# Kernel tuning notes

Measured on AMD Instinct MI355X. Metric: run time of the kernel, lower is better.

Reference implementation:

```python
import jax, jax.numpy as jnp
import numpy as np

BETA = 5.5
MEM_FILLED = 25  # number of occupied slots per class; remaining slots are zero (empty)


def setup_inputs() -> dict:
    key = jax.random.key(0)
    ks = jax.random.split(key, 7)
    C, M, D = 1000, 50, 1024
    mem = jax.random.normal(ks[0], (C, M, D), jnp.float32)
    # emulate a partially-filled memory bank: slots >= MEM_FILLED are empty (all-zero rows)
    mem = mem * (jnp.arange(M)[None, :, None] < MEM_FILLED)
    return {
        "img_feat": jax.random.normal(ks[1], (1, D), jnp.float32),
        "image_feature_memory": mem,
        "fixed_global_feat_vanilla": jax.random.normal(ks[2], (C, 1, D), jnp.float32),
        "global_bias": 0.01 * jax.random.normal(ks[3], (C, D), jnp.float32),
        "global_bias_key": 0.01 * jax.random.normal(ks[4], (C, D), jnp.float32),
        "global_bias_value": 0.01 * jax.random.normal(ks[5], (C, D), jnp.float32),
        "global_ffn_bias": 0.01 * jax.random.normal(ks[6], (C, D), jnp.float32),
        "logit_scale": jnp.asarray(np.log(100.0), dtype=jnp.float32),
    }


def _l2norm(x, axis=-1):
    return x / jnp.linalg.norm(x, axis=axis, keepdims=True)


def reference(img_feat, image_feature_memory, fixed_global_feat_vanilla,
              global_bias, global_bias_key, global_bias_value,
              global_ffn_bias, logit_scale):
    # DualMem.get_image_pred, args.position == 'all', similarity_weighted classifier
    sg = jax.lax.stop_gradient  # torch.no_grad() block
    mem = jnp.concatenate([image_feature_memory, fixed_global_feat_vanilla], axis=1)  # (C, M+1, D)

    q = img_feat + jnp.mean(global_bias, axis=0, keepdims=True)      # (1, D)
    K = mem + global_bias_key[:, None, :]                             # (C, M+1, D)
    V = mem + global_bias_value[:, None, :]                           # (C, M+1, D)

    empty = (jnp.sum(mem, axis=-1) == 0)[..., None]                   # (C, M+1, 1) empty slots
    Kn = jnp.where(empty, 0.0, _l2norm(K))
    Vn = jnp.where(empty, 0.0, _l2norm(V))
    qn = _l2norm(q)
    qn, Kn, Vn = sg(qn), sg(Kn), sg(Vn)

    sim = jnp.exp(-BETA * (1.0 - jnp.einsum('d,cmd->cm', qn[0], Kn)))  # (C, M+1)
    adaptive = jnp.einsum('cm,cmd->cd', sim, Vn)                       # (C, D)
    adaptive = _l2norm(adaptive)
    adaptive = adaptive[None] + global_ffn_bias[None]                  # (1, C, D) position in {'output','all'}
    adaptive = _l2norm(adaptive)

    logits = jnp.exp(logit_scale) * jnp.einsum('bcd,bd->bc', adaptive, img_feat)  # (1, C)
    return jax.nn.softmax(logits, axis=1)
```

## Files before the change

kernel.cpp:

```cpp
#include <hip/hip_runtime.h>
#include <math.h>

#define BETA 5.5f
#define NC 1000
#define NM 51
#define ND 1024

__device__ __forceinline__ float wave_reduce_sum(float v) {
#pragma unroll
    for (int off = 32; off >= 1; off >>= 1) v += __shfl_xor(v, off, 64);
    return v;
}

__device__ __forceinline__ float block_reduce_sum(float v, float* red, int w, int lane) {
    v = wave_reduce_sum(v);
    __syncthreads();
    if (lane == 0) red[w] = v;
    __syncthreads();
    return red[0] + red[1] + red[2] + red[3];
}

__global__ __launch_bounds__(128) void colsum_kernel(const float* __restrict__ gb,
                                                     float* __restrict__ qsum) {
    int d = blockIdx.x * 128 + threadIdx.x;
    int c0 = blockIdx.y * 125;
    const float* p = gb + (size_t)c0 * ND + d;
    float s = 0.f;
    for (int c = 0; c < 125; ++c) s += p[(size_t)c * ND];
    atomicAdd(&qsum[d], s);
}

__global__ __launch_bounds__(256) void dualmem_main(
    const float* __restrict__ img,
    const float* __restrict__ mem,
    const float* __restrict__ fixedg,
    const float* __restrict__ qsum,
    const float* __restrict__ gbk,
    const float* __restrict__ gbv,
    const float* __restrict__ ffn,
    const float* __restrict__ lsp,
    float* __restrict__ logits)
{
    __shared__ float lds_acc[4 * ND];
    __shared__ float red[8];

    const int c = blockIdx.x;
    const int t = threadIdx.x;
    const int w = t >> 6;
    const int lane = t & 63;

    float4 qn[4];
    float ssq = 0.f;
#pragma unroll
    for (int j = 0; j < 4; ++j) {
        float4 iv = ((const float4*)img)[j * 64 + lane];
        float4 sv = ((const float4*)qsum)[j * 64 + lane];
        float4 qv;
        qv.x = iv.x + sv.x * (1.f / NC);
        qv.y = iv.y + sv.y * (1.f / NC);
        qv.z = iv.z + sv.z * (1.f / NC);
        qv.w = iv.w + sv.w * (1.f / NC);
        ssq += qv.x * qv.x + qv.y * qv.y + qv.z * qv.z + qv.w * qv.w;
        qn[j] = qv;
    }
    ssq = wave_reduce_sum(ssq);
    float qrn = rsqrtf(ssq);
#pragma unroll
    for (int j = 0; j < 4; ++j) {
        qn[j].x *= qrn; qn[j].y *= qrn; qn[j].z *= qrn; qn[j].w *= qrn;
    }

    const float* bkp = gbk + (size_t)c * ND;
    const float* bvp = gbv + (size_t)c * ND;
    float4 bk[4], bv[4], acc[4];
#pragma unroll
    for (int j = 0; j < 4; ++j) {
        bk[j] = ((const float4*)bkp)[j * 64 + lane];
        bv[j] = ((const float4*)bvp)[j * 64 + lane];
        acc[j] = make_float4(0.f, 0.f, 0.f, 0.f);
    }

    for (int m = w; m < NM; m += 4) {
        const float* row = (m < 50) ? mem + ((size_t)c * 50 + m) * ND
                                    : fixedg + (size_t)c * ND;
        float4 mv[4];
        float sm = 0.f, ssqK = 0.f, dotK = 0.f, ssqV = 0.f;
#pragma unroll
        for (int j = 0; j < 4; ++j) {
            float4 v = ((const float4*)row)[j * 64 + lane];
            mv[j] = v;
            sm += v.x + v.y + v.z + v.w;
            float kx = v.x + bk[j].x, ky = v.y + bk[j].y, kz = v.z + bk[j].z, kw = v.w + bk[j].w;
            ssqK += kx * kx + ky * ky + kz * kz + kw * kw;
            dotK += qn[j].x * kx + qn[j].y * ky + qn[j].z * kz + qn[j].w * kw;
            float vx = v.x + bv[j].x, vy = v.y + bv[j].y, vz = v.z + bv[j].z, vw = v.w + bv[j].w;
            ssqV += vx * vx + vy * vy + vz * vz + vw * vw;
        }
        sm   = wave_reduce_sum(sm);
        ssqK = wave_reduce_sum(ssqK);
        dotK = wave_reduce_sum(dotK);
        ssqV = wave_reduce_sum(ssqV);
        if (sm != 0.f) {
            float simv = expf(-BETA * (1.f - dotK * rsqrtf(ssqK)));
            float wt = simv * rsqrtf(ssqV);
#pragma unroll
            for (int j = 0; j < 4; ++j) {
                acc[j].x += wt * (mv[j].x + bv[j].x);
                acc[j].y += wt * (mv[j].y + bv[j].y);
                acc[j].z += wt * (mv[j].z + bv[j].z);
                acc[j].w += wt * (mv[j].w + bv[j].w);
            }
        }
    }

#pragma unroll
    for (int j = 0; j < 4; ++j)
        ((float4*)lds_acc)[w * 256 + j * 64 + lane] = acc[j];
    __syncthreads();

    float4 a = make_float4(0.f, 0.f, 0.f, 0.f);
#pragma unroll
    for (int wv = 0; wv < 4; ++wv) {
        float4 p = ((float4*)lds_acc)[wv * 256 + t];
        a.x += p.x; a.y += p.y; a.z += p.z; a.w += p.w;
    }

    float ssqA = block_reduce_sum(a.x * a.x + a.y * a.y + a.z * a.z + a.w * a.w, red, w, lane);
    float arn = rsqrtf(ssqA);
    float4 fv = ((const float4*)(ffn + (size_t)c * ND))[t];
    a.x = a.x * arn + fv.x;
    a.y = a.y * arn + fv.y;
    a.z = a.z * arn + fv.z;
    a.w = a.w * arn + fv.w;
    float ssqB = block_reduce_sum(a.x * a.x + a.y * a.y + a.z * a.z + a.w * a.w, red, w, lane);
    float brn = rsqrtf(ssqB);

    float4 iv = ((const float4*)img)[t];
    float dp = a.x * iv.x + a.y * iv.y + a.z * iv.z + a.w * iv.w;
    dp = block_reduce_sum(dp, red, w, lane);

    if (t == 0) logits[c] = expf(lsp[0]) * dp * brn;
}

__global__ __launch_bounds__(256) void softmax_kernel(const float* __restrict__ logits,
                                                      float* __restrict__ out) {
    __shared__ float red[8];
    int t = threadIdx.x, w = t >> 6, lane = t & 63;
    float l[4];
#pragma unroll
    for (int i = 0; i < 4; ++i) {
        int idx = t * 4 + i;
        l[i] = (idx < NC) ? logits[idx] : -3.402823466e+38f;
    }
    float mx = fmaxf(fmaxf(l[0], l[1]), fmaxf(l[2], l[3]));
#pragma unroll
    for (int off = 32; off >= 1; off >>= 1) mx = fmaxf(mx, __shfl_xor(mx, off, 64));
    __syncthreads();
    if (lane == 0) red[w] = mx;
    __syncthreads();
    mx = fmaxf(fmaxf(red[0], red[1]), fmaxf(red[2], red[3]));
    __syncthreads();

    float e[4], s = 0.f;
#pragma unroll
    for (int i = 0; i < 4; ++i) {
        int idx = t * 4 + i;
        e[i] = (idx < NC) ? expf(l[i] - mx) : 0.f;
        s += e[i];
    }
    s = block_reduce_sum(s, red, w, lane);
    float inv = 1.f / s;
#pragma unroll
    for (int i = 0; i < 4; ++i) {
        int idx = t * 4 + i;
        if (idx < NC) out[idx] = e[i] * inv;
    }
}

extern "C" void kernel_launch(void* const* d_in, const int* in_sizes, int n_in,
                              void* d_out, int out_size, void* d_ws, size_t ws_size,
                              hipStream_t stream) {
    const float* img    = (const float*)d_in[0];
    const float* mem    = (const float*)d_in[1];
    const float* fixedg = (const float*)d_in[2];
    const float* gb     = (const float*)d_in[3];
    const float* gbk    = (const float*)d_in[4];
    const float* gbv    = (const float*)d_in[5];
    const float* ffn    = (const float*)d_in[6];
    const float* ls     = (const float*)d_in[7];

    float* ws     = (float*)d_ws;
    float* qsum   = ws;
    float* logits = ws + 1024;
    float* out    = (float*)d_out;

    hipMemsetAsync(qsum, 0, ND * sizeof(float), stream);
    colsum_kernel<<<dim3(8, 8), 128, 0, stream>>>(gb, qsum);
    dualmem_main<<<NC, 256, 0, stream>>>(img, mem, fixedg, qsum, gbk, gbv, ffn, ls, logits);
    softmax_kernel<<<1, 256, 0, stream>>>(logits, out);
}
```

Baseline: 331.5 us.

## Split each class across two blocks, add finalize kernel, nontemporal memory loads

The main kernel now launches two blocks per class, each handling half of the memory slots. Each block writes its partial accumulator to workspace, and a new finalize kernel sums the two halves and does the normalisations and logit. The column-sum atomic plus memset is replaced by per-block partial sums that every block reduces on load. Memory rows are read with nontemporal loads. The aim is more parallelism and fewer wasted waves, since each wave previously looped about 13 times per class. The cost is an extra kernel launch and an 8 MB round trip through workspace for the partial accumulators.

```diff
diff --git a/kernel.cpp b/kernel.cpp
--- a/kernel.cpp
+++ b/kernel.cpp
@@ -6,6 +6,8 @@
 #define NM 51
 #define ND 1024
 
+typedef float nt_float4 __attribute__((ext_vector_type(4)));
+
 __device__ __forceinline__ float wave_reduce_sum(float v) {
 #pragma unroll
     for (int off = 32; off >= 1; off >>= 1) v += __shfl_xor(v, off, 64);
@@ -21,40 +23,44 @@
 }
 
 __global__ __launch_bounds__(128) void colsum_kernel(const float* __restrict__ gb,
-                                                     float* __restrict__ qsum) {
+                                                     float* __restrict__ qpart) {
     int d = blockIdx.x * 128 + threadIdx.x;
     int c0 = blockIdx.y * 125;
     const float* p = gb + (size_t)c0 * ND + d;
     float s = 0.f;
     for (int c = 0; c < 125; ++c) s += p[(size_t)c * ND];
-    atomicAdd(&qsum[d], s);
+    qpart[blockIdx.y * ND + d] = s;
 }
 
 __global__ __launch_bounds__(256) void dualmem_main(
     const float* __restrict__ img,
     const float* __restrict__ mem,
     const float* __restrict__ fixedg,
-    const float* __restrict__ qsum,
+    const float* __restrict__ qpart,
     const float* __restrict__ gbk,
     const float* __restrict__ gbv,
-    const float* __restrict__ ffn,
-    const float* __restrict__ lsp,
-    float* __restrict__ logits)
+    float* __restrict__ accpart)
 {
     __shared__ float lds_acc[4 * ND];
-    __shared__ float red[8];
-
-    const int c = blockIdx.x;
+
+    const int c = blockIdx.x >> 1;
+    const int half = blockIdx.x & 1;
     const int t = threadIdx.x;
     const int w = t >> 6;
     const int lane = t & 63;
+    const int ww = half * 4 + w;
 
     float4 qn[4];
     float ssq = 0.f;
 #pragma unroll
     for (int j = 0; j < 4; ++j) {
+        float4 sv = make_float4(0.f, 0.f, 0.f, 0.f);
+#pragma unroll
+        for (int p = 0; p < 8; ++p) {
+            float4 pv = ((const float4*)qpart)[p * 256 + j * 64 + lane];
+            sv.x += pv.x; sv.y += pv.y; sv.z += pv.z; sv.w += pv.w;
+        }
         float4 iv = ((const float4*)img)[j * 64 + lane];
-        float4 sv = ((const float4*)qsum)[j * 64 + lane];
         float4 qv;
         qv.x = iv.x + sv.x * (1.f / NC);
         qv.y = iv.y + sv.y * (1.f / NC);
@@ -80,14 +86,14 @@
         acc[j] = make_float4(0.f, 0.f, 0.f, 0.f);
     }
 
-    for (int m = w; m < NM; m += 4) {
-        const float* row = (m < 50) ? mem + ((size_t)c * 50 + m) * ND
-                                    : fixedg + (size_t)c * ND;
-        float4 mv[4];
+    for (int m = ww; m < NM; m += 8) {
+        const nt_float4* row = (m < 50) ? (const nt_float4*)(mem + ((size_t)c * 50 + m) * ND)
+                                        : (const nt_float4*)(fixedg + (size_t)c * ND);
+        nt_float4 mv[4];
         float sm = 0.f, ssqK = 0.f, dotK = 0.f, ssqV = 0.f;
 #pragma unroll
         for (int j = 0; j < 4; ++j) {
-            float4 v = ((const float4*)row)[j * 64 + lane];
+            nt_float4 v = __builtin_nontemporal_load(&row[j * 64 + lane]);
             mv[j] = v;
             sm += v.x + v.y + v.z + v.w;
             float kx = v.x + bk[j].x, ky = v.y + bk[j].y, kz = v.z + bk[j].z, kw = v.w + bk[j].w;
@@ -124,6 +130,26 @@
         float4 p = ((float4*)lds_acc)[wv * 256 + t];
         a.x += p.x; a.y += p.y; a.z += p.z; a.w += p.w;
     }
+    ((float4*)(accpart + (size_t)blockIdx.x * ND))[t] = a;
+}
+
+__global__ __launch_bounds__(256) void finalize_kernel(
+    const float* __restrict__ img,
+    const float* __restrict__ accpart,
+    const float* __restrict__ ffn,
+    const float* __restrict__ lsp,
+    float* __restrict__ logits)
+{
+    __shared__ float red[8];
+    const int c = blockIdx.x;
+    const int t = threadIdx.x;
+    const int w = t >> 6;
+    const int lane = t & 63;
+
+    float4 a0 = ((const float4*)(accpart + (size_t)(2 * c) * ND))[t];
+    float4 a1 = ((const float4*)(accpart + (size_t)(2 * c + 1) * ND))[t];
+    float4 a;
+    a.x = a0.x + a1.x; a.y = a0.y + a1.y; a.z = a0.z + a1.z; a.w = a0.w + a1.w;
 
     float ssqA = block_reduce_sum(a.x * a.x + a.y * a.y + a.z * a.z + a.w * a.w, red, w, lane);
     float arn = rsqrtf(ssqA);
@@ -189,13 +215,14 @@
     const float* ffn    = (const float*)d_in[6];
     const float* ls     = (const float*)d_in[7];
 
-    float* ws     = (float*)d_ws;
-    float* qsum   = ws;
-    float* logits = ws + 1024;
-    float* out    = (float*)d_out;
-
-    hipMemsetAsync(qsum, 0, ND * sizeof(float), stream);
-    colsum_kernel<<<dim3(8, 8), 128, 0, stream>>>(gb, qsum);
-    dualmem_main<<<NC, 256, 0, stream>>>(img, mem, fixedg, qsum, gbk, gbv, ffn, ls, logits);
+    float* ws      = (float*)d_ws;
+    float* qpart   = ws;
+    float* accpart = ws + 8 * ND;
+    float* logits  = accpart + 2000 * ND;
+    float* out     = (float*)d_out;
+
+    colsum_kernel<<<dim3(8, 8), 128, 0, stream>>>(gb, qpart);
+    dualmem_main<<<2 * NC, 256, 0, stream>>>(img, mem, fixedg, qpart, gbk, gbv, accpart);
+    finalize_kernel<<<NC, 256, 0, stream>>>(img, accpart, ffn, ls, logits);
     softmax_kernel<<<1, 256, 0, stream>>>(logits, out);
 }
```

New measurement: 318.7 us (median of 2 runs). -3.9%, faster.
